# Optimization experiments

Measured on AMD Instinct MI355X. Metric: run time of the kernel, lower is better.

## Reference

```python
import jax, jax.numpy as jnp
import numpy as np

D = 256; H = 8; L = 4; K = 4; AS = 2; HD = D // H
KK = K * K
LEVEL_SHAPES = [(128, 128), (64, 64), (32, 32), (16, 16)]


def _kernel_indices():
    # kernel_size=4 (even): linspace(-1.5, 1.5, 4); stack [j, i] then / K
    idx = jnp.linspace(-1.5, 1.5, K)
    ii, jj = jnp.meshgrid(idx, idx, indexing='ij')
    return jnp.stack([jj, ii], axis=-1).reshape(-1, 2) / K  # (KK, 2)


def _bilinear(vf, g, Hl, Wl):
    # vf: (b, H, Hl*Wl, HD) per-level value; g: (b, l1, H, KK, 2) in [0,1]
    # grid_sample semantics, align_corners=False, zero padding
    b, l1, h, kk, _ = g.shape
    x = g[..., 0] * Wl - 0.5
    y = g[..., 1] * Hl - 0.5
    x0 = jnp.floor(x)
    y0 = jnp.floor(y)
    acc = None
    for dx, dy in ((0, 0), (1, 0), (0, 1), (1, 1)):
        xi = x0 + dx
        yi = y0 + dy
        w = (1.0 - jnp.abs(x - xi)) * (1.0 - jnp.abs(y - yi))
        valid = (xi >= 0) & (xi < Wl) & (yi >= 0) & (yi < Hl)
        idx = (jnp.clip(yi, 0, Hl - 1) * Wl + jnp.clip(xi, 0, Wl - 1)).astype(jnp.int32)
        idx = idx.transpose(0, 2, 1, 3).reshape(b, h, l1 * kk)
        gth = jnp.take_along_axis(vf, idx[..., None], axis=2)  # (b,H,l1*kk,HD)
        ww = (w * valid).transpose(0, 2, 1, 3).reshape(b, h, l1 * kk)
        c = gth * ww[..., None]
        acc = c if acc is None else acc + c
    return acc.reshape(b, h, l1, kk, HD).transpose(0, 2, 1, 3, 4)  # (b,l1,H,kk,HD)


def setup_inputs() -> dict:
    key = jax.random.key(0)
    ks = jax.random.split(key, 9)
    b, l1 = 4, 1024
    l2 = sum(h * w for h, w in LEVEL_SHAPES)  # 21760
    query = jax.random.normal(ks[0], (b, l1, D), jnp.float32)
    value = jax.random.normal(ks[1], (b, l2, D), jnp.float32)
    centers = jax.random.uniform(ks[2], (b, l1, 2), jnp.float32)
    sizes = jax.random.uniform(ks[3], (b, l1, 2), jnp.float32) * 0.2 + 0.05
    ref_windows = jnp.concatenate([centers, sizes], axis=-1)  # (b,l1,4) cx,cy,w,h
    s = 1.0 / np.sqrt(D)
    Wv = jax.random.normal(ks[4], (D, D), jnp.float32) * s
    bv = jnp.zeros((D,), jnp.float32)
    Wo = jax.random.normal(ks[5], (D, D), jnp.float32) * s
    bo = jnp.zeros((D,), jnp.float32)
    Wbox = jax.random.normal(ks[6], (L * H * 4, D), jnp.float32) * 0.01
    bbox = jax.random.uniform(ks[7], (H * L * 4,), jnp.float32)
    Wattn = jax.random.normal(ks[8], (H * L * AS * AS, D), jnp.float32) * s
    battn = jnp.zeros((H * L * AS * AS,), jnp.float32)
    v_shape = np.array(LEVEL_SHAPES, np.int64)
    starts = np.cumsum([0] + [h * w for h, w in LEVEL_SHAPES[:-1]])
    v_start_index = np.array(starts, np.int64)
    v_mask = jnp.zeros((b, l2), bool)
    return dict(query=query, value=value, ref_windows=ref_windows, Wv=Wv, bv=bv,
                Wo=Wo, bo=bo, Wbox=Wbox, bbox=bbox, Wattn=Wattn, battn=battn,
                v_shape=v_shape, v_start_index=v_start_index, v_mask=v_mask)


def reference(query, value, ref_windows, Wv, bv, Wo, bo, Wbox, bbox, Wattn, battn,
              v_shape, v_start_index, v_mask):
    b, l1, _ = query.shape
    l2 = value.shape[1]
    # value projection + padding mask
    v = value @ Wv.T + bv
    v = jnp.where(v_mask[..., None], 0.0, v).reshape(b, l2, H, HD)
    # where to attend: offset boxes -> sampling grid (normalizer=None branch)
    off = (query @ Wbox.T + bbox).reshape(b, l1, H, L, 4)
    refw = ref_windows[:, :, None, None, :]            # (b,l1,1,1,4)
    refsz = jnp.concatenate([refw[..., 2:4], refw[..., 2:4]], axis=-1)
    boxes = refw + off / 8.0 * refsz                   # (b,l1,H,L,4)
    center = boxes[..., None, :2]
    size = boxes[..., None, 2:]
    grid = center + _kernel_indices() * jax.nn.relu(size)  # (b,l1,H,L,KK,2)
    # attention weights (attn_size grid upsampled to kernel_size by repeat_interleave)
    aw = (query @ Wattn.T + battn).reshape(b, l1, H, L, AS, AS)
    nr = K // AS
    aw = jnp.repeat(jnp.repeat(aw, nr, axis=-1), nr, axis=-2)  # (b,l1,H,L,K,K)
    sw = jax.nn.softmax(aw.reshape(b, l1, H, -1), axis=-1).reshape(b, l1, H, L, KK)
    lw = jax.nn.softmax(aw, axis=3).reshape(b, l1, H, L, KK)
    out = jnp.zeros((b, l1, H, HD), query.dtype)
    mout = jnp.zeros((b, l1, H, HD), query.dtype)
    for li in range(L):
        Hl, Wl = int(v_shape[li, 0]), int(v_shape[li, 1])
        st = int(v_start_index[li])
        vf = v[:, st:st + Hl * Wl].transpose(0, 2, 1, 3)  # (b,H,Hl*Wl,HD)
        samp = _bilinear(vf, grid[:, :, :, li], Hl, Wl)   # (b,l1,H,KK,HD)
        out = out + jnp.einsum('bqhkd,bqhk->bqhd', samp, sw[:, :, :, li])
        mout = mout + jnp.einsum('bqhkd,bqhk->bqhd', samp, lw[:, :, :, li])
    out = out.reshape(b, l1, D) @ Wo.T + bo
    mout = mout.reshape(b, l1, D) @ Wo.T + bo
    return out, mout, aw
```

## Files before the change

kernel.cpp:

```cpp
#include <hip/hip_runtime.h>
#include <hip/hip_bf16.h>
#include <hip/hip_fp16.h>


typedef __attribute__((ext_vector_type(8))) short short8;
typedef __attribute__((ext_vector_type(4))) float f32x4;
typedef __attribute__((ext_vector_type(4))) unsigned int uint4v;

__device__ __forceinline__ unsigned short f2bf(float f) {
    unsigned int u = __float_as_uint(f);
    unsigned int r = u + 0x7FFFu + ((u >> 16) & 1u);
    return (unsigned short)(r >> 16);
}
__device__ __forceinline__ unsigned short f2h(float f) {
    __half h = __float2half_rn(f);
    return *reinterpret_cast<unsigned short*>(&h);
}
__device__ __forceinline__ unsigned int pkbf(float a, float b) {
    __hip_bfloat162 h = __float22bfloat162_rn(float2{a, b});
    return *reinterpret_cast<unsigned int*>(&h);
}
__device__ __forceinline__ short8 pack2(float4 x, float4 y) {
    uint4v u;
    u[0] = pkbf(x.x, x.y); u[1] = pkbf(x.z, x.w);
    u[2] = pkbf(y.x, y.y); u[3] = pkbf(y.z, y.w);
    return __builtin_bit_cast(short8, u);
}
__device__ __forceinline__ void gld_lds16(const float* g, float* l) {
    __builtin_amdgcn_global_load_lds(
        (const __attribute__((address_space(1))) unsigned int*)g,
        (__attribute__((address_space(3))) unsigned int*)l, 16, 0, 0);
}

#define TILE_F 4096

__device__ __forceinline__ void gemm_body_v(
    const float* __restrict__ A, const float* __restrict__ W,
    const float* __restrict__ bias, unsigned short* __restrict__ C,
    int bm, int bn, int vb, int pbase, float* AsF, float* WsF)
{
    const int tid  = threadIdx.x;
    const int lane = tid & 63;
    const int wave = tid >> 6;
    const int wm = (wave & 1) * 64;
    const int wn = (wave >> 1) * 64;
    const int kg = lane >> 4;
    const int lm = lane & 15;

    f32x4 acc[4][4];
#pragma unroll
    for (int i = 0; i < 4; ++i)
#pragma unroll
        for (int j = 0; j < 4; ++j) {
            acc[i][j][0] = 0.f; acc[i][j][1] = 0.f;
            acc[i][j][2] = 0.f; acc[i][j][3] = 0.f;
        }

    const int g = (lane & 7) ^ (lane >> 3);
    const float* Ag = A + (size_t)(bm + 32 * wave + (lane >> 3)) * 256 + 4 * g;
    const float* Wg = W + (size_t)(bn + 32 * wave + (lane >> 3)) * 256 + 4 * g;
    const int ldsw = (32 * wave) * 32;

    const int p0 = (2 * kg) ^ (lm & 7);
    const int p1 = p0 ^ 1;
    const int abase = (wm + lm) * 8;
    const int bbase = (wn + lm) * 8;

#define STAGE_VQ(BUF, K0)                                                     \
    {                                                                         \
        _Pragma("unroll")                                                     \
        for (int j = 0; j < 4; ++j) {                                         \
            gld_lds16(Ag + (size_t)j * 8 * 256 + (K0),                        \
                      AsF + (BUF) * TILE_F + ldsw + j * 8 * 32);              \
            gld_lds16(Wg + (size_t)j * 8 * 256 + (K0),                        \
                      WsF + (BUF) * TILE_F + ldsw + j * 8 * 32);              \
        }                                                                     \
    }

#define COMPUTE_VQ(BUF)                                                       \
    {                                                                         \
        const float4* Af4 = (const float4*)(AsF + (BUF) * TILE_F);            \
        const float4* Wf4 = (const float4*)(WsF + (BUF) * TILE_F);            \
        short8 af[4], bfr[4];                                                 \
        _Pragma("unroll")                                                     \
        for (int i = 0; i < 4; ++i) {                                         \
            float4 c0 = Af4[abase + i * 128 + p0];                            \
            float4 c1 = Af4[abase + i * 128 + p1];                            \
            af[i] = pack2(c0, c1);                                            \
        }                                                                     \
        _Pragma("unroll")                                                     \
        for (int j = 0; j < 4; ++j) {                                         \
            float4 c0 = Wf4[bbase + j * 128 + p0];                            \
            float4 c1 = Wf4[bbase + j * 128 + p1];                            \
            bfr[j] = pack2(c0, c1);                                           \
        }                                                                     \
        _Pragma("unroll")                                                     \
        for (int i = 0; i < 4; ++i)                                           \
            _Pragma("unroll")                                                 \
            for (int j = 0; j < 4; ++j)                                       \
                acc[i][j] = __builtin_amdgcn_mfma_f32_16x16x32_bf16(          \
                    af[i], bfr[j], acc[i][j], 0, 0, 0);                       \
    }

    STAGE_VQ(0, 0)
    asm volatile("s_waitcnt vmcnt(0)" ::: "memory");
    __builtin_amdgcn_s_barrier();

#pragma unroll 2
    for (int it = 0; it < 8; ++it) {
        const int cur = it & 1;
        const int nxt = cur ^ 1;
        if (it < 7) STAGE_VQ(nxt, 32 * (it + 1))
        COMPUTE_VQ(cur)
        if (it < 7) {
            asm volatile("s_waitcnt vmcnt(0) lgkmcnt(0)" ::: "memory");
            __builtin_amdgcn_s_barrier();
            asm volatile("" ::: "memory");
        }
    }
#undef STAGE_VQ
#undef COMPUTE_VQ

    __syncthreads();
    {
        unsigned short* sv = (unsigned short*)AsF;
#pragma unroll
        for (int j = 0; j < 4; ++j) {
            const int cb = wn + j * 16;
            const int pl = cb >> 5;
            const int ch = (cb & 16) + lm;
            const float bcol = bias[bn + cb + lm];
#pragma unroll
            for (int i = 0; i < 4; ++i) {
#pragma unroll
                for (int r = 0; r < 4; ++r) {
                    const int px = wm + i * 16 + kg * 4 + r;
                    sv[(pl * 128 + px) * 32 + ch] = f2h(acc[i][j][r] + bcol);
                }
            }
        }
    }
    __syncthreads();
    {
        const unsigned short* sv = (const unsigned short*)AsF;
        const int plbase = vb * 8 + (bn >> 5);
#pragma unroll
        for (int q = 0; q < 8; ++q) {
            size_t gbase = ((size_t)(plbase + (q >> 1)) * 21760 + pbase) * 32
                         + (q & 1) * 2048 + tid * 8;
            *(uint4v*)&C[gbase] = *(const uint4v*)&sv[q * 2048 + tid * 8];
        }
    }
}

#define LDA 56

__device__ __forceinline__ void gemm_body_f32(
    const float* __restrict__ A, const float* __restrict__ W,
    const float* __restrict__ bias, float* __restrict__ C,
    int N, int bm, int bn, unsigned short* As, unsigned short* Ws)
{
    const int tid  = threadIdx.x;
    const int lane = tid & 63;
    const int wave = tid >> 6;
    const int wm = (wave & 1) * 64;
    const int wn = (wave >> 1) * 64;
    const int lr = tid >> 1;
    const int lh = (tid & 1) * 16;
    const int kg = lane >> 4;
    const int lm = lane & 15;

    f32x4 acc[4][4];
#pragma unroll
    for (int i = 0; i < 4; ++i)
#pragma unroll
        for (int j = 0; j < 4; ++j) {
            acc[i][j][0] = 0.f; acc[i][j][1] = 0.f;
            acc[i][j][2] = 0.f; acc[i][j][3] = 0.f;
        }

    const float* Ap = A + (size_t)(bm + lr) * 256 + lh;
    const float* Wp = W + (size_t)(bn + lr) * 256 + lh;
    unsigned short* Asp = &As[lr * LDA + lh];
    unsigned short* Wsp = &Ws[lr * LDA + lh];

    for (int k0 = 0; k0 < 256; k0 += 32) {
        float4 a0 = *(const float4*)(Ap + k0);
        float4 a1 = *(const float4*)(Ap + k0 + 4);
        float4 a2 = *(const float4*)(Ap + k0 + 8);
        float4 a3 = *(const float4*)(Ap + k0 + 12);
        float4 w0 = *(const float4*)(Wp + k0);
        float4 w1 = *(const float4*)(Wp + k0 + 4);
        float4 w2 = *(const float4*)(Wp + k0 + 8);
        float4 w3 = *(const float4*)(Wp + k0 + 12);
        __syncthreads();
        *(short8*)(Asp)     = pack2(a0, a1);
        *(short8*)(Asp + 8) = pack2(a2, a3);
        *(short8*)(Wsp)     = pack2(w0, w1);
        *(short8*)(Wsp + 8) = pack2(w2, w3);
        __syncthreads();
        short8 af[4], bfr[4];
#pragma unroll
        for (int i = 0; i < 4; ++i)
            af[i] = *(const short8*)&As[(wm + i * 16 + lm) * LDA + kg * 8];
#pragma unroll
        for (int j = 0; j < 4; ++j)
            bfr[j] = *(const short8*)&Ws[(wn + j * 16 + lm) * LDA + kg * 8];
#pragma unroll
        for (int i = 0; i < 4; ++i)
#pragma unroll
            for (int j = 0; j < 4; ++j)
                acc[i][j] = __builtin_amdgcn_mfma_f32_16x16x32_bf16(
                    af[i], bfr[j], acc[i][j], 0, 0, 0);
    }

#pragma unroll
    for (int j = 0; j < 4; ++j) {
        int col = bn + wn + j * 16 + lm;
        float bcol = bias[col];
#pragma unroll
        for (int i = 0; i < 4; ++i)
#pragma unroll
            for (int r = 0; r < 4; ++r) {
                int row = bm + wm + i * 16 + kg * 4 + r;
                C[(size_t)row * N + col] = acc[i][j][r] + bcol;
            }
    }
}

__device__ __forceinline__ void gemm_body_bf16A(
    const unsigned short* __restrict__ A, const float* __restrict__ W,
    const float* __restrict__ bias, float* __restrict__ C,
    int N, int bm, int bn, unsigned short* As, unsigned short* Ws)
{
    const int tid  = threadIdx.x;
    const int lane = tid & 63;
    const int wave = tid >> 6;
    const int wm = (wave & 1) * 64;
    const int wn = (wave >> 1) * 64;
    const int lr = tid >> 1;
    const int lh = (tid & 1) * 16;
    const int kg = lane >> 4;
    const int lm = lane & 15;

    f32x4 acc[4][4];
#pragma unroll
    for (int i = 0; i < 4; ++i)
#pragma unroll
        for (int j = 0; j < 4; ++j) {
            acc[i][j][0] = 0.f; acc[i][j][1] = 0.f;
            acc[i][j][2] = 0.f; acc[i][j][3] = 0.f;
        }

    const unsigned short* Ap = A + (size_t)(bm + lr) * 256 + lh;
    const float* Wp = W + (size_t)(bn + lr) * 256 + lh;
    unsigned short* Asp = &As[lr * LDA + lh];
    unsigned short* Wsp = &Ws[lr * LDA + lh];

    for (int k0 = 0; k0 < 256; k0 += 32) {
        uint4v a01 = *(const uint4v*)(Ap + k0);
        uint4v a23 = *(const uint4v*)(Ap + k0 + 8);
        float4 w0 = *(const float4*)(Wp + k0);
        float4 w1 = *(const float4*)(Wp + k0 + 4);
        float4 w2 = *(const float4*)(Wp + k0 + 8);
        float4 w3 = *(const float4*)(Wp + k0 + 12);
        __syncthreads();
        *(short8*)(Asp)     = __builtin_bit_cast(short8, a01);
        *(short8*)(Asp + 8) = __builtin_bit_cast(short8, a23);
        *(short8*)(Wsp)     = pack2(w0, w1);
        *(short8*)(Wsp + 8) = pack2(w2, w3);
        __syncthreads();
        short8 af[4], bfr[4];
#pragma unroll
        for (int i = 0; i < 4; ++i)
            af[i] = *(const short8*)&As[(wm + i * 16 + lm) * LDA + kg * 8];
#pragma unroll
        for (int j = 0; j < 4; ++j)
            bfr[j] = *(const short8*)&Ws[(wn + j * 16 + lm) * LDA + kg * 8];
#pragma unroll
        for (int i = 0; i < 4; ++i)
#pragma unroll
            for (int j = 0; j < 4; ++j)
                acc[i][j] = __builtin_amdgcn_mfma_f32_16x16x32_bf16(
                    af[i], bfr[j], acc[i][j], 0, 0, 0);
    }

#pragma unroll
    for (int j = 0; j < 4; ++j) {
        int col = bn + wn + j * 16 + lm;
        float bcol = bias[col];
#pragma unroll
        for (int i = 0; i < 4; ++i)
#pragma unroll
            for (int r = 0; r < 4; ++r) {
                int row = bm + wm + i * 16 + kg * 4 + r;
                C[(size_t)row * N + col] = acc[i][j][r] + bcol;
            }
    }
}

__global__ __launch_bounds__(256) void gemm_vq_kernel(
    const float* __restrict__ value, const float* __restrict__ Wv,
    const float* __restrict__ bv, unsigned short* __restrict__ v,
    const float* __restrict__ query,
    const float* __restrict__ Wbox, const float* __restrict__ bbox, float* __restrict__ off,
    const float* __restrict__ Wattn, const float* __restrict__ battn, float* __restrict__ awr)
{
    __shared__ __align__(16) char smem[65536];
    const int x = blockIdx.x;
    if (x < 1360) {
        const int rb = (x >> 4) * 8 + (x & 7);
        const int s  = (x >> 3) & 1;
        const int vb = rb / 170;
        const int pbase = (rb - vb * 170) * 128;
        gemm_body_v(value, Wv, bv, v, rb * 128, s * 128,
                    vb, pbase, (float*)smem, (float*)(smem + 32768));
    } else {
        const int idx = x - 1360;
        const int bm = (idx & 31) * 128;
        unsigned short* As = (unsigned short*)smem;
        unsigned short* Ws = As + 128 * LDA;
        if (idx < 32) gemm_body_f32(query, Wbox, bbox, off, 128, bm, 0, As, Ws);
        else          gemm_body_f32(query, Wattn, battn, awr, 128, bm, 0, As, Ws);
    }
}

__global__ __launch_bounds__(256) void gemm_o_kernel(
    const unsigned short* __restrict__ A, const float* __restrict__ W,
    const float* __restrict__ bias, float* __restrict__ C)
{
    __shared__ __align__(16) unsigned short As[128 * LDA];
    __shared__ __align__(16) unsigned short Ws[128 * LDA];
    gemm_body_bf16A(A, W, bias, C, 256, blockIdx.x * 128, blockIdx.y * 128, As, Ws);
}

__global__ __launch_bounds__(256) void sample_kernel(
    const unsigned short* __restrict__ v, const float* __restrict__ off,
    const float* __restrict__ awr, const float* __restrict__ refw,
    float* __restrict__ aw_out, unsigned short* __restrict__ accb)
{
    const int x   = blockIdx.x;
    const int cls = x & 7;
    const int b   = cls >> 1;
    const int hg  = cls & 1;
    const int bq  = (b << 10) | (x >> 3);
    const int t   = threadIdx.x;

    __shared__ float ref4[4];
    __shared__ float awl[64];
    __shared__ float bxs[64];
    __shared__ float swl[256];
    __shared__ float lwl[256];
    __shared__ int4  tp[16 * 66];

    if (t < 4)  ref4[t] = refw[bq * 4 + t];
    if (t < 64) awl[t] = awr[(size_t)bq * 128 + hg * 64 + t];
    __syncthreads();

    if (t < 64) {
        float o = off[(size_t)bq * 128 + hg * 64 + t];
        int comp = t & 3;
        float r0 = ref4[0], r1 = ref4[1], r2 = ref4[2], r3 = ref4[3];
        float bx;
        if (comp == 0)      bx = r0 + o * 0.125f * r2;
        else if (comp == 1) bx = r1 + o * 0.125f * r3;
        else if (comp == 2) bx = r2 + o * 0.125f * r2;
        else                bx = r3 + o * 0.125f * r3;
        bxs[t] = bx;

        const int hp = t >> 4, r = t & 15;
        float a = awl[t];
        float m = a;
#pragma unroll
        for (int s = 1; s < 16; s <<= 1) m = fmaxf(m, __shfl_xor(m, s, 16));
        float se = expf(a - m);
#pragma unroll
        for (int s = 1; s < 16; s <<= 1) se += __shfl_xor(se, s, 16);
        const float inv_s = 1.0f / (4.0f * se);

        float* awq = aw_out + (size_t)bq * 512 + (4 * hg + hp) * 64;
#pragma unroll
        for (int j = 0; j < 4; ++j) {
            int eidx = r * 4 + j;
            int l  = eidx >> 4;
            int ky = (eidx >> 2) & 3;
            int kx = eidx & 3;
            int pos = (ky >> 1) * 2 + (kx >> 1);
            float raw = awl[hp * 16 + l * 4 + pos];
            swl[hp * 64 + eidx] = expf(raw - m) * inv_s;
            int base = hp * 16 + pos;
            float m2 = awl[base];
#pragma unroll
            for (int li = 1; li < 4; ++li) m2 = fmaxf(m2, awl[base + li * 4]);
            float s2 = 0.f;
#pragma unroll
            for (int li = 0; li < 4; ++li) s2 += expf(awl[base + li * 4] - m2);
            lwl[hp * 64 + eidx] = expf(raw - m2) / s2;
            awq[eidx] = raw;
        }
    }
    __syncthreads();

    {
        const int STs_[4] = {0, 16384, 20480, 21504};
        int e = t;
        int hp = e >> 6, rem = e & 63, l = rem >> 4, kk = rem & 15;
        const float* bx = &bxs[hp * 16 + l * 4];
        float cx = bx[0], cy = bx[1];
        float bw = fmaxf(bx[2], 0.f), bh = fmaxf(bx[3], 0.f);
        float kx = -0.375f + 0.25f * (float)(kk & 3);
        float ky = -0.375f + 0.25f * (float)(kk >> 2);
        int Wl = 128 >> l;
        float xg = (cx + kx * bw) * (float)Wl - 0.5f;
        float yg = (cy + ky * bh) * (float)Wl - 0.5f;
        float x0f = floorf(xg), y0f = floorf(yg);
        int x0 = (int)x0f, y0 = (int)y0f;
        float fx = xg - x0f, fy = yg - y0f;
        float sww = swl[e], lww = lwl[e];
        int rowbase = (b * 8 + 4 * hg + hp) * 21760 + STs_[l];
        int4* dst = &tp[(hp * 4 + l) * 66 + kk * 4];
#pragma unroll
        for (int tap = 0; tap < 4; ++tap) {
            int dx = tap & 1, dy = tap >> 1;
            int xi = x0 + dx, yi = y0 + dy;
            float w = (dx ? fx : 1.f - fx) * (dy ? fy : 1.f - fy);
            if (xi < 0 || xi >= Wl || yi < 0 || yi >= Wl) w = 0.f;
            int xc = min(max(xi, 0), Wl - 1);
            int yc = min(max(yi, 0), Wl - 1);
            unsigned int uo = f2h(w * sww);
            unsigned int um = f2h(w * lww);
            dst[tap] = int4{(rowbase + yc * Wl + xc) << 3,
                            (int)(uo | (uo << 16)),
                            (int)(um | (um << 16)), 0};
        }
    }
    __syncthreads();

    const int hp   = t >> 6;
    const int lane = t & 63;
    const int l    = (lane >> 4) & 3;
    const int sub  = (lane >> 3) & 1;
    const int cl   = lane & 7;
    const uint2* vp = (const uint2*)v;
    const int4* sp = &tp[(hp * 4 + l) * 66 + sub];

    float a0 = 0.f, a1 = 0.f, a2 = 0.f, a3 = 0.f;
    float m0 = 0.f, m1 = 0.f, m2 = 0.f, m3 = 0.f;
#pragma unroll
    for (int oo = 0; oo < 4; ++oo) {
        __half2 zero2 = __float2half2_rn(0.f);
        __half2 ao0 = zero2, ao1 = zero2, am0 = zero2, am1 = zero2;
#pragma unroll
        for (int i = 0; i < 8; ++i) {
            int4 d = sp[2 * (oo * 8 + i)];
            uint2 pv = vp[(size_t)(d.x + cl)];
            __half2 va = __builtin_bit_cast(__half2, pv.x);
            __half2 vb = __builtin_bit_cast(__half2, pv.y);
            __half2 wo = __builtin_bit_cast(__half2, d.y);
            __half2 wm = __builtin_bit_cast(__half2, d.z);
            ao0 = __hfma2(va, wo, ao0); ao1 = __hfma2(vb, wo, ao1);
            am0 = __hfma2(va, wm, am0); am1 = __hfma2(vb, wm, am1);
        }
        float2 f;
        f = __half22float2(ao0); a0 += f.x; a1 += f.y;
        f = __half22float2(ao1); a2 += f.x; a3 += f.y;
        f = __half22float2(am0); m0 += f.x; m1 += f.y;
        f = __half22float2(am1); m2 += f.x; m3 += f.y;
    }
#pragma unroll
    for (int s = 8; s <= 32; s <<= 1) {
        a0 += __shfl_xor(a0, s); a1 += __shfl_xor(a1, s);
        a2 += __shfl_xor(a2, s); a3 += __shfl_xor(a3, s);
        m0 += __shfl_xor(m0, s); m1 += __shfl_xor(m1, s);
        m2 += __shfl_xor(m2, s); m3 += __shfl_xor(m3, s);
    }
    if (lane < 8) {
        size_t base = (size_t)bq * 256 + (4 * hg + hp) * 32 + cl * 4;
        *(uint2*)&accb[base] = uint2{pkbf(a0, a1), pkbf(a2, a3)};
        *(uint2*)&accb[base + (size_t)4096 * 256] = uint2{pkbf(m0, m1), pkbf(m2, m3)};
    }
}

extern "C" void kernel_launch(void* const* d_in, const int* in_sizes, int n_in,
                              void* d_out, int out_size, void* d_ws, size_t ws_size,
                              hipStream_t stream) {
    const float* query = (const float*)d_in[0];
    const float* value = (const float*)d_in[1];
    const float* refw  = (const float*)d_in[2];
    const float* Wv    = (const float*)d_in[3];
    const float* bv    = (const float*)d_in[4];
    const float* Wo    = (const float*)d_in[5];
    const float* bo    = (const float*)d_in[6];
    const float* Wbox  = (const float*)d_in[7];
    const float* bbox  = (const float*)d_in[8];
    const float* Wattn = (const float*)d_in[9];
    const float* battn = (const float*)d_in[10];

    float* out = (float*)d_out;
    float* aw_out = out + 2 * 1048576;

    unsigned short* v = (unsigned short*)d_ws;
    float* off = (float*)((char*)d_ws + 44564480);
    float* awr = off + 524288;
    unsigned short* accb = (unsigned short*)(awr + 524288);

    gemm_vq_kernel<<<1424, 256, 0, stream>>>(value, Wv, bv, v,
                                             query, Wbox, bbox, off,
                                             Wattn, battn, awr);
    sample_kernel<<<8192, 256, 0, stream>>>(v, off, awr, refw, aw_out, accb);
    gemm_o_kernel<<<dim3(64, 2), 256, 0, stream>>>(accb, Wo, bo, out);
}
```

Baseline: 236.7 us.

## Load value-projection weights straight into registers instead of staging through LDS

In the value-projection GEMM, the weight tile is no longer copied into shared memory. Each thread now prefetches its own weight fragments from global memory into registers one k-step ahead and packs them to bf16 for the MFMA. Only the activation tile is still double-buffered in LDS. This halves the fused kernel's shared-memory footprint, which should allow more resident blocks per CU. In exchange it costs extra VGPRs and narrower per-lane global reads of the small weight matrix, which is likely cache-resident.

```diff
diff --git a/kernel.cpp b/kernel.cpp
--- a/kernel.cpp
+++ b/kernel.cpp
@@ -37,7 +37,7 @@
 __device__ __forceinline__ void gemm_body_v(
     const float* __restrict__ A, const float* __restrict__ W,
     const float* __restrict__ bias, unsigned short* __restrict__ C,
-    int bm, int bn, int vb, int pbase, float* AsF, float* WsF)
+    int bm, int bn, int vb, int pbase, float* AsF)
 {
     const int tid  = threadIdx.x;
     const int lane = tid & 63;
@@ -58,51 +58,34 @@
 
     const int g = (lane & 7) ^ (lane >> 3);
     const float* Ag = A + (size_t)(bm + 32 * wave + (lane >> 3)) * 256 + 4 * g;
-    const float* Wg = W + (size_t)(bn + 32 * wave + (lane >> 3)) * 256 + 4 * g;
     const int ldsw = (32 * wave) * 32;
 
     const int p0 = (2 * kg) ^ (lm & 7);
     const int p1 = p0 ^ 1;
     const int abase = (wm + lm) * 8;
-    const int bbase = (wn + lm) * 8;
-
-#define STAGE_VQ(BUF, K0)                                                     \
+
+    const float* Wrow = W + (size_t)(bn + wn + lm) * 256 + kg * 8;
+
+#define STAGE_A(BUF, K0)                                                      \
+    {                                                                         \
+        _Pragma("unroll")                                                     \
+        for (int j = 0; j < 4; ++j)                                           \
+            gld_lds16(Ag + (size_t)j * 8 * 256 + (K0),                        \
+                      AsF + (BUF) * TILE_F + ldsw + j * 8 * 32);              \
+    }
+#define LOAD_W(K0)                                                            \
     {                                                                         \
         _Pragma("unroll")                                                     \
         for (int j = 0; j < 4; ++j) {                                         \
-            gld_lds16(Ag + (size_t)j * 8 * 256 + (K0),                        \
-                      AsF + (BUF) * TILE_F + ldsw + j * 8 * 32);              \
-            gld_lds16(Wg + (size_t)j * 8 * 256 + (K0),                        \
-                      WsF + (BUF) * TILE_F + ldsw + j * 8 * 32);              \
+            fw[j][0] = *(const float4*)(Wrow + j * 4096 + (K0));              \
+            fw[j][1] = *(const float4*)(Wrow + j * 4096 + (K0) + 4);          \
         }                                                                     \
     }
 
-#define COMPUTE_VQ(BUF)                                                       \
-    {                                                                         \
-        const float4* Af4 = (const float4*)(AsF + (BUF) * TILE_F);            \
-        const float4* Wf4 = (const float4*)(WsF + (BUF) * TILE_F);            \
-        short8 af[4], bfr[4];                                                 \
-        _Pragma("unroll")                                                     \
-        for (int i = 0; i < 4; ++i) {                                         \
-            float4 c0 = Af4[abase + i * 128 + p0];                            \
-            float4 c1 = Af4[abase + i * 128 + p1];                            \
-            af[i] = pack2(c0, c1);                                            \
-        }                                                                     \
-        _Pragma("unroll")                                                     \
-        for (int j = 0; j < 4; ++j) {                                         \
-            float4 c0 = Wf4[bbase + j * 128 + p0];                            \
-            float4 c1 = Wf4[bbase + j * 128 + p1];                            \
-            bfr[j] = pack2(c0, c1);                                           \
-        }                                                                     \
-        _Pragma("unroll")                                                     \
-        for (int i = 0; i < 4; ++i)                                           \
-            _Pragma("unroll")                                                 \
-            for (int j = 0; j < 4; ++j)                                       \
-                acc[i][j] = __builtin_amdgcn_mfma_f32_16x16x32_bf16(          \
-                    af[i], bfr[j], acc[i][j], 0, 0, 0);                       \
-    }
-
-    STAGE_VQ(0, 0)
+    float4 fw[4][2];
+
+    STAGE_A(0, 0)
+    LOAD_W(0)
     asm volatile("s_waitcnt vmcnt(0)" ::: "memory");
     __builtin_amdgcn_s_barrier();
 
@@ -110,16 +93,33 @@
     for (int it = 0; it < 8; ++it) {
         const int cur = it & 1;
         const int nxt = cur ^ 1;
-        if (it < 7) STAGE_VQ(nxt, 32 * (it + 1))
-        COMPUTE_VQ(cur)
+        if (it < 7) STAGE_A(nxt, 32 * (it + 1))
+        short8 bfr[4];
+#pragma unroll
+        for (int j = 0; j < 4; ++j) bfr[j] = pack2(fw[j][0], fw[j][1]);
+        if (it < 7) LOAD_W(32 * (it + 1))
+        const float4* Af4 = (const float4*)(AsF + cur * TILE_F);
+        short8 af[4];
+#pragma unroll
+        for (int i = 0; i < 4; ++i) {
+            float4 c0 = Af4[abase + i * 128 + p0];
+            float4 c1 = Af4[abase + i * 128 + p1];
+            af[i] = pack2(c0, c1);
+        }
+#pragma unroll
+        for (int i = 0; i < 4; ++i)
+#pragma unroll
+            for (int j = 0; j < 4; ++j)
+                acc[i][j] = __builtin_amdgcn_mfma_f32_16x16x32_bf16(
+                    af[i], bfr[j], acc[i][j], 0, 0, 0);
         if (it < 7) {
             asm volatile("s_waitcnt vmcnt(0) lgkmcnt(0)" ::: "memory");
             __builtin_amdgcn_s_barrier();
             asm volatile("" ::: "memory");
         }
     }
-#undef STAGE_VQ
-#undef COMPUTE_VQ
+#undef STAGE_A
+#undef LOAD_W
 
     __syncthreads();
     {
@@ -306,7 +306,7 @@
     const float* __restrict__ Wbox, const float* __restrict__ bbox, float* __restrict__ off,
     const float* __restrict__ Wattn, const float* __restrict__ battn, float* __restrict__ awr)
 {
-    __shared__ __align__(16) char smem[65536];
+    __shared__ __align__(16) char smem[32768];
     const int x = blockIdx.x;
     if (x < 1360) {
         const int rb = (x >> 4) * 8 + (x & 7);
@@ -314,7 +314,7 @@
         const int vb = rb / 170;
         const int pbase = (rb - vb * 170) * 128;
         gemm_body_v(value, Wv, bv, v, rb * 128, s * 128,
-                    vb, pbase, (float*)smem, (float*)(smem + 32768));
+                    vb, pbase, (float*)smem);
     } else {
         const int idx = x - 1360;
         const int bm = (idx & 31) * 128;
```

Result: slower. 263.3 us (+11.2%).
